# Kernel optimization log

Hardware: AMD Instinct MI355X
Metric: run time of the kernel (lower is better)

## Reference

```python
import jax, jax.numpy as jnp
import numpy as np

B, S, H = 2, 2048, 2048
INTER = 1024
N_ROUTED = 8
ZERO = 4
TOTAL = N_ROUTED + ZERO
TOP_K = 2
SCALE = 1.5


def setup_inputs() -> dict:
    key = jax.random.key(0)
    k0, k1, k2, k3, k4, k5 = jax.random.split(key, 6)
    w = 0.02  # weight init scale
    return {
        "hidden_states": jax.random.normal(k0, (B, S, H), jnp.float32),
        "classifier_w": jax.random.normal(k1, (TOTAL, H), jnp.float32) * w,
        "e_score_correction_bias": jax.random.normal(k2, (TOTAL,), jnp.float32) * w,
        "gate_w": jax.random.normal(k3, (N_ROUTED, INTER, H), jnp.float32) * w,
        "up_w": jax.random.normal(k4, (N_ROUTED, INTER, H), jnp.float32) * w,
        "down_w": jax.random.normal(k5, (N_ROUTED, H, INTER), jnp.float32) * w,
    }


def reference(hidden_states, classifier_w, e_score_correction_bias, gate_w, up_w, down_w):
    x = hidden_states  # [B,S,H]
    total = classifier_w.shape[0]
    n_routed = gate_w.shape[0]

    # --- Router: softmax over all experts, bias only for selection ---
    logits = jnp.einsum('bsh,eh->bse', x, classifier_w)          # [B,S,total]
    probs = jax.nn.softmax(logits, axis=-1)
    biased = probs + e_score_correction_bias
    _, idx = jax.lax.top_k(biased, TOP_K)                         # [B,S,K] int
    rw = jnp.take_along_axis(probs, idx, axis=-1) * SCALE         # unbiased probs as weights

    # Dense per-expert weight via one-hot combine (Equal+Mul+ReduceSum in original)
    w_full = jnp.sum(jax.nn.one_hot(idx, total, dtype=x.dtype) * rw[..., None], axis=-2)  # [B,S,total]

    # --- Compute ALL routed experts densely (matches original op graph) ---
    g = jnp.einsum('bsh,eih->bsei', x, gate_w)                    # [B,S,E,INTER]
    u = jnp.einsum('bsh,eih->bsei', x, up_w)
    act = jax.nn.silu(g) * u
    expert_out = jnp.einsum('bsei,ehi->bseh', act, down_w)        # [B,S,E,H]

    out = jnp.einsum('bse,bseh->bsh', w_full[..., :n_routed], expert_out)
    # Zero (identity) experts pass hidden_states through
    out = out + x * jnp.sum(w_full[..., n_routed:], axis=-1, keepdims=True)
    return out
```

## Files before the change

### kernel.cpp

```cpp
#include <hip/hip_runtime.h>
#include <cstdint>

#define T_TOKENS 4096
#define HDIM 2048
#define IDIM 1024
#define NEXP 8
#define NTOT 12
#define MAX_SLOTS 8320

typedef __bf16 bf16x8_t __attribute__((ext_vector_type(8)));
typedef float f32x4_t __attribute__((ext_vector_type(4)));
typedef unsigned short u16x8_t __attribute__((ext_vector_type(8)));

__device__ __forceinline__ unsigned short f2bf(float f) {
    unsigned int u = __builtin_bit_cast(unsigned int, f);
    u += 0x7fffu + ((u >> 16) & 1u);
    return (unsigned short)(u >> 16);
}
__device__ __forceinline__ float bfu2f(unsigned short u) {
    unsigned int v = ((unsigned int)u) << 16;
    return __builtin_bit_cast(float, v);
}
__device__ __forceinline__ void async16(const unsigned short* g, unsigned short* l) {
    __builtin_amdgcn_global_load_lds(
        (const unsigned int __attribute__((address_space(1)))*)g,
        (unsigned int __attribute__((address_space(3)))*)l,
        16, 0, 0);
}
__device__ __forceinline__ void cvt16(const float* src, unsigned short* dst) {
    f32x4_t f0 = ((const f32x4_t*)src)[0];
    f32x4_t f1 = ((const f32x4_t*)src)[1];
    f32x4_t f2 = ((const f32x4_t*)src)[2];
    f32x4_t f3 = ((const f32x4_t*)src)[3];
    u16x8_t a, b;
#pragma unroll
    for (int j = 0; j < 4; ++j) { a[j] = f2bf(f0[j]); a[4 + j] = f2bf(f1[j]); }
#pragma unroll
    for (int j = 0; j < 4; ++j) { b[j] = f2bf(f2[j]); b[4 + j] = f2bf(f3[j]); }
    ((u16x8_t*)dst)[0] = a;
    ((u16x8_t*)dst)[1] = b;
}

__global__ void init_kernel(int* __restrict__ meta) {
    int i = threadIdx.x;
    if (i < 32) meta[i] = 0;
}

__global__ void noop_kernel() {}

__global__ void router_kernel(const float* __restrict__ x,
                              const float* __restrict__ cw,
                              const float* __restrict__ bias,
                              int* __restrict__ counts,
                              int* __restrict__ tok_e,
                              float* __restrict__ tok_w,
                              float* __restrict__ zero_w) {
    const int token = blockIdx.x;
    const int ln = threadIdx.x;
    const float* xr = x + (size_t)token * HDIM;
    float acc[NTOT];
#pragma unroll
    for (int e = 0; e < NTOT; ++e) acc[e] = 0.f;
    for (int h0 = ln * 4; h0 < HDIM; h0 += 256) {
        f32x4_t xv = *(const f32x4_t*)(xr + h0);
#pragma unroll
        for (int e = 0; e < NTOT; ++e) {
            f32x4_t wv = *(const f32x4_t*)(cw + e * HDIM + h0);
            acc[e] += xv[0] * wv[0] + xv[1] * wv[1] + xv[2] * wv[2] + xv[3] * wv[3];
        }
    }
#pragma unroll
    for (int e = 0; e < NTOT; ++e) {
        float v = acc[e];
#pragma unroll
        for (int s = 32; s > 0; s >>= 1) v += __shfl_xor(v, s, 64);
        acc[e] = v;
    }
    if (ln == 0) {
        float mx = acc[0];
#pragma unroll
        for (int e = 1; e < NTOT; ++e) mx = fmaxf(mx, acc[e]);
        float p[NTOT];
        float sum = 0.f;
#pragma unroll
        for (int e = 0; e < NTOT; ++e) { p[e] = __expf(acc[e] - mx); sum += p[e]; }
        float inv = 1.f / sum;
#pragma unroll
        for (int e = 0; e < NTOT; ++e) p[e] *= inv;
        float b[NTOT];
#pragma unroll
        for (int e = 0; e < NTOT; ++e) b[e] = p[e] + bias[e];
        int i0 = 0; float v0 = b[0];
#pragma unroll
        for (int e = 1; e < NTOT; ++e) if (b[e] > v0) { v0 = b[e]; i0 = e; }
        int i1 = -1; float v1 = -3.0e38f;
#pragma unroll
        for (int e = 0; e < NTOT; ++e) if (e != i0 && b[e] > v1) { v1 = b[e]; i1 = e; }
        if (i1 < 0) i1 = (i0 == 0) ? 1 : 0;
        float w0 = p[i0] * 1.5f, w1 = p[i1] * 1.5f;
        tok_e[2 * token] = i0; tok_e[2 * token + 1] = i1;
        tok_w[2 * token] = w0; tok_w[2 * token + 1] = w1;
        float zw = 0.f;
        if (i0 >= NEXP) zw += w0; else atomicAdd(&counts[i0], 1);
        if (i1 >= NEXP) zw += w1; else atomicAdd(&counts[i1], 1);
        zero_w[token] = zw;
    }
}

__global__ void scan_kernel(const int* __restrict__ counts, int* __restrict__ offs) {
    if (threadIdx.x == 0 && blockIdx.x == 0) {
        int a = 0;
        for (int e = 0; e < NEXP; ++e) {
            offs[e] = a;
            int c = counts[e];
            if (c < 0) c = 0;
            if (c > T_TOKENS) c = T_TOKENS;
            a += c;
        }
        if (a > 2 * T_TOKENS) a = 2 * T_TOKENS;
        offs[NEXP] = a;
    }
}

__global__ void place_kernel(const int* __restrict__ tok_e, const float* __restrict__ tok_w,
                             const int* __restrict__ offs, int* __restrict__ fill,
                             int* __restrict__ token_list, float* __restrict__ slot_w,
                             int* __restrict__ map) {
    int token = blockIdx.x * blockDim.x + threadIdx.x;
    if (token >= T_TOKENS) return;
#pragma unroll
    for (int j = 0; j < 2; ++j) {
        int e = tok_e[2 * token + j];
        int m = -1;
        if (e >= 0 && e < NEXP) {
            int pos = atomicAdd(&fill[e], 1);
            int slot = offs[e] + pos;
            if (slot >= 0 && slot < 2 * T_TOKENS) {
                token_list[slot] = token;
                slot_w[slot] = tok_w[2 * token + j];
                m = slot;
            }
        }
        map[2 * token + j] = m;
    }
}

__launch_bounds__(256, 2)
__global__ void gemm1_kernel(const float* __restrict__ x,
                             const float* __restrict__ gate_w,
                             const float* __restrict__ up_w,
                             const int* __restrict__ offs,
                             const int* __restrict__ token_list,
                             const float* __restrict__ slot_w,
                             unsigned short* __restrict__ act) {
    const int e = blockIdx.z;
    const int off = offs[e];
    int Me = offs[e + 1] - off;
    if (Me < 0) Me = 0;
    if (Me > T_TOKENS) Me = T_TOKENS;
    const int m0 = blockIdx.y * 128;
    if (m0 >= Me) return;
    const int n0 = blockIdx.x * 128;

    __shared__ __align__(16) unsigned short As[128][32];
    __shared__ __align__(16) unsigned short Gs[128][32];
    __shared__ __align__(16) unsigned short Us[128][32];

    const int tid = threadIdx.x;
    const int srow = tid >> 1;
    const int shalf = (tid & 1) * 16;

    int tr = m0 + srow; if (tr >= Me) tr = Me - 1;
    int tok = token_list[off + tr];
    if (tok < 0 || tok >= T_TOKENS) tok = 0;
    const float* aA = x + (size_t)tok * HDIM + shalf;
    const float* aG = gate_w + (size_t)e * IDIM * HDIM + (size_t)(n0 + srow) * HDIM + shalf;
    const float* aU = up_w + (size_t)e * IDIM * HDIM + (size_t)(n0 + srow) * HDIM + shalf;
    unsigned short* lA = &As[srow][shalf];
    unsigned short* lG = &Gs[srow][shalf];
    unsigned short* lU = &Us[srow][shalf];

    const int wv = tid >> 6, ln = tid & 63;
    const int wm = wv & 1, wn = wv >> 1;
    const int fr = ln & 15;
    const int fk = (ln >> 4) * 8;

    f32x4_t accg[4][4] = {};
    f32x4_t accu[4][4] = {};

    for (int k0 = 0; k0 < HDIM; k0 += 32) {
        cvt16(aA + k0, lA);
        cvt16(aG + k0, lG);
        cvt16(aU + k0, lU);
        __syncthreads();
        bf16x8_t af[4], gf[4], uf[4];
#pragma unroll
        for (int t = 0; t < 4; ++t) {
            af[t] = *(const bf16x8_t*)&As[wm * 64 + t * 16 + fr][fk];
            gf[t] = *(const bf16x8_t*)&Gs[wn * 64 + t * 16 + fr][fk];
            uf[t] = *(const bf16x8_t*)&Us[wn * 64 + t * 16 + fr][fk];
        }
#pragma unroll
        for (int mt = 0; mt < 4; ++mt)
#pragma unroll
            for (int nt = 0; nt < 4; ++nt) {
                accg[mt][nt] = __builtin_amdgcn_mfma_f32_16x16x32_bf16(af[mt], gf[nt], accg[mt][nt], 0, 0, 0);
                accu[mt][nt] = __builtin_amdgcn_mfma_f32_16x16x32_bf16(af[mt], uf[nt], accu[mt][nt], 0, 0, 0);
            }
        __syncthreads();
    }

#pragma unroll
    for (int mt = 0; mt < 4; ++mt) {
#pragma unroll
        for (int r = 0; r < 4; ++r) {
            int rloc = wm * 64 + mt * 16 + (ln >> 4) * 4 + r;
            int grow = m0 + rloc;
            if (grow < Me) {
                float w = slot_w[off + grow];
                size_t rb = (size_t)(off + grow) * IDIM + n0;
#pragma unroll
                for (int nt = 0; nt < 4; ++nt) {
                    float g = accg[mt][nt][r];
                    float u = accu[mt][nt][r];
                    float s = g / (1.f + __expf(-g));
                    act[rb + wn * 64 + nt * 16 + fr] = f2bf(s * u * w);
                }
            }
        }
    }
}

__launch_bounds__(256, 2)
__global__ void gemm2_kernel(const unsigned short* __restrict__ act,
                             const float* __restrict__ dwn,
                             const int* __restrict__ offs,
                             unsigned short* __restrict__ dout) {
    const int e = blockIdx.z;
    const int off = offs[e];
    int Me = offs[e + 1] - off;
    if (Me < 0) Me = 0;
    if (Me > T_TOKENS) Me = T_TOKENS;
    const int m0 = blockIdx.y * 128;
    if (m0 >= Me) return;
    const int n0 = blockIdx.x * 128;

    __shared__ __align__(16) unsigned short As[128][32];
    __shared__ __align__(16) unsigned short Bs[128][32];

    const int tid = threadIdx.x;
    const int wv = tid >> 6, ln = tid & 63;

    const int sr0 = wv * 16 + (ln >> 2);
    const int sc = (ln & 3) * 8;
    int ar0 = off + m0 + sr0;      if (ar0 >= MAX_SLOTS) ar0 = MAX_SLOTS - 1;
    int ar1 = off + m0 + 64 + sr0; if (ar1 >= MAX_SLOTS) ar1 = MAX_SLOTS - 1;
    const unsigned short* aA0 = act + (size_t)ar0 * IDIM + sc;
    const unsigned short* aA1 = act + (size_t)ar1 * IDIM + sc;
    unsigned short* lA0 = &As[wv * 16][0];
    unsigned short* lA1 = &As[64 + wv * 16][0];

    const int srow = tid >> 1;
    const int shalf = (tid & 1) * 16;
    const float* aB = dwn + (size_t)e * HDIM * IDIM + (size_t)(n0 + srow) * IDIM + shalf;
    unsigned short* lB = &Bs[srow][shalf];

    const int wm = wv & 1, wn = wv >> 1;
    const int fr = ln & 15;
    const int fk = (ln >> 4) * 8;

    f32x4_t acc[4][4] = {};

    for (int k0 = 0; k0 < IDIM; k0 += 32) {
        async16(aA0 + k0, lA0);
        async16(aA1 + k0, lA1);
        cvt16(aB + k0, lB);
        __syncthreads();
        bf16x8_t af[4], bfr[4];
#pragma unroll
        for (int t = 0; t < 4; ++t) {
            af[t] = *(const bf16x8_t*)&As[wm * 64 + t * 16 + fr][fk];
            bfr[t] = *(const bf16x8_t*)&Bs[wn * 64 + t * 16 + fr][fk];
        }
#pragma unroll
        for (int mt = 0; mt < 4; ++mt)
#pragma unroll
            for (int nt = 0; nt < 4; ++nt)
                acc[mt][nt] = __builtin_amdgcn_mfma_f32_16x16x32_bf16(af[mt], bfr[nt], acc[mt][nt], 0, 0, 0);
        __syncthreads();
    }

#pragma unroll
    for (int mt = 0; mt < 4; ++mt) {
#pragma unroll
        for (int r = 0; r < 4; ++r) {
            int rloc = wm * 64 + mt * 16 + (ln >> 4) * 4 + r;
            int grow = m0 + rloc;
            if (grow < Me) {
                size_t rb = (size_t)(off + grow) * HDIM + n0;
#pragma unroll
                for (int nt = 0; nt < 4; ++nt)
                    dout[rb + wn * 64 + nt * 16 + fr] = f2bf(acc[mt][nt][r]);
            }
        }
    }
}

__global__ void finalize_kernel(const float* __restrict__ x,
                                const unsigned short* __restrict__ dout,
                                const int* __restrict__ map,
                                const float* __restrict__ zero_w,
                                float* __restrict__ out) {
    int gid = blockIdx.x * blockDim.x + threadIdx.x;
    int token = gid >> 8;
    int hg = (gid & 255) * 8;
    int s0 = map[2 * token], s1 = map[2 * token + 1];
    float zw = zero_w[token];
    size_t base = (size_t)token * HDIM + hg;
    f32x4_t x0 = *(const f32x4_t*)(x + base);
    f32x4_t x1 = *(const f32x4_t*)(x + base + 4);
    float o[8];
#pragma unroll
    for (int j = 0; j < 4; ++j) { o[j] = zw * x0[j]; o[4 + j] = zw * x1[j]; }
    if (s0 >= 0 && s0 < 2 * T_TOKENS) {
        u16x8_t d = *(const u16x8_t*)(dout + (size_t)s0 * HDIM + hg);
#pragma unroll
        for (int j = 0; j < 8; ++j) o[j] += bfu2f(d[j]);
    }
    if (s1 >= 0 && s1 < 2 * T_TOKENS) {
        u16x8_t d = *(const u16x8_t*)(dout + (size_t)s1 * HDIM + hg);
#pragma unroll
        for (int j = 0; j < 8; ++j) o[j] += bfu2f(d[j]);
    }
    f32x4_t o0, o1;
#pragma unroll
    for (int j = 0; j < 4; ++j) { o0[j] = o[j]; o1[j] = o[4 + j]; }
    *(f32x4_t*)(out + base) = o0;
    *(f32x4_t*)(out + base + 4) = o1;
}

extern "C" void kernel_launch(void* const* d_in, const int* in_sizes, int n_in,
                              void* d_out, int out_size, void* d_ws, size_t ws_size,
                              hipStream_t stream) {
    const float* x = (const float*)d_in[0];
    const float* cw = (const float*)d_in[1];
    const float* bias = (const float*)d_in[2];
    const float* gw = (const float*)d_in[3];
    const float* uw = (const float*)d_in[4];
    const float* dw = (const float*)d_in[5];
    float* out = (float*)d_out;

    char* ws = (char*)d_ws;
    int* counts = (int*)(ws + 0);
    int* fill = (int*)(ws + 32);
    int* offs = (int*)(ws + 64);
    int* tok_e = (int*)(ws + 128);
    float* tok_w = (float*)(ws + 32896);
    float* zero_w = (float*)(ws + 65664);
    int* map = (int*)(ws + 82048);
    int* token_list = (int*)(ws + 114816);
    float* slot_w = (float*)(ws + 148096);
    unsigned short* act = (unsigned short*)(ws + 181504);
    unsigned short* dout = (unsigned short*)(ws + 181504 + 17039360);
    const size_t needed = 181504ull + 17039360ull + 34078720ull;
    if (ws_size < needed) {
        noop_kernel<<<1, 64, 0, stream>>>();
        return;
    }

    init_kernel<<<1, 64, 0, stream>>>((int*)ws);

    router_kernel<<<T_TOKENS, 64, 0, stream>>>(x, cw, bias, counts, tok_e, tok_w, zero_w);
    scan_kernel<<<1, 64, 0, stream>>>(counts, offs);
    place_kernel<<<(T_TOKENS + 255) / 256, 256, 0, stream>>>(tok_e, tok_w, offs, fill,
                                                             token_list, slot_w, map);
    gemm1_kernel<<<dim3(IDIM / 128, 32, NEXP), 256, 0, stream>>>(x, gw, uw, offs,
                                                                 token_list, slot_w, act);
    gemm2_kernel<<<dim3(HDIM / 128, 32, NEXP), 256, 0, stream>>>(act, dw, offs, dout);
    finalize_kernel<<<(T_TOKENS * HDIM / 8 + 255) / 256, 256, 0, stream>>>(x, dout, map,
                                                                           zero_w, out);
}
```

Measured before the change: 517.9 us.

## Double-buffer LDS staging and shrink M tile to 64 in expert GEMMs

Both expert GEMM kernels now use double-buffered shared memory: the next K slice is loaded from global memory and converted while the current slice feeds the MFMAs, leaving one barrier per iteration. The M tile drops from 128 to 64 rows, with each wave covering 32 columns, and the launch grid grows to match. This should hide global load latency and cut padding waste for experts with few tokens. The cost is lower data reuse per block (the fp32 weights are re-read and re-converted for twice as many M tiles) and more register pressure from prefetched values.

```diff
diff --git a/kernel.cpp b/kernel.cpp
--- a/kernel.cpp
+++ b/kernel.cpp
@@ -11,6 +11,7 @@
 typedef __bf16 bf16x8_t __attribute__((ext_vector_type(8)));
 typedef float f32x4_t __attribute__((ext_vector_type(4)));
 typedef unsigned short u16x8_t __attribute__((ext_vector_type(8)));
+typedef unsigned int u32x4_t __attribute__((ext_vector_type(4)));
 
 __device__ __forceinline__ unsigned short f2bf(float f) {
     unsigned int u = __builtin_bit_cast(unsigned int, f);
@@ -20,25 +21,23 @@
 __device__ __forceinline__ float bfu2f(unsigned short u) {
     unsigned int v = ((unsigned int)u) << 16;
     return __builtin_bit_cast(float, v);
+}
+__device__ __forceinline__ unsigned int pk2(float a, float b) {
+    return (unsigned int)f2bf(a) | ((unsigned int)f2bf(b) << 16);
+}
+__device__ __forceinline__ void pack8(f32x4_t f0, f32x4_t f1, unsigned short* dst) {
+    u32x4_t v;
+    v[0] = pk2(f0[0], f0[1]);
+    v[1] = pk2(f0[2], f0[3]);
+    v[2] = pk2(f1[0], f1[1]);
+    v[3] = pk2(f1[2], f1[3]);
+    *(u32x4_t*)dst = v;
 }
 __device__ __forceinline__ void async16(const unsigned short* g, unsigned short* l) {
     __builtin_amdgcn_global_load_lds(
         (const unsigned int __attribute__((address_space(1)))*)g,
         (unsigned int __attribute__((address_space(3)))*)l,
         16, 0, 0);
-}
-__device__ __forceinline__ void cvt16(const float* src, unsigned short* dst) {
-    f32x4_t f0 = ((const f32x4_t*)src)[0];
-    f32x4_t f1 = ((const f32x4_t*)src)[1];
-    f32x4_t f2 = ((const f32x4_t*)src)[2];
-    f32x4_t f3 = ((const f32x4_t*)src)[3];
-    u16x8_t a, b;
-#pragma unroll
-    for (int j = 0; j < 4; ++j) { a[j] = f2bf(f0[j]); a[4 + j] = f2bf(f1[j]); }
-#pragma unroll
-    for (int j = 0; j < 4; ++j) { b[j] = f2bf(f2[j]); b[4 + j] = f2bf(f3[j]); }
-    ((u16x8_t*)dst)[0] = a;
-    ((u16x8_t*)dst)[1] = b;
 }
 
 __global__ void init_kernel(int* __restrict__ meta) {
@@ -158,52 +157,71 @@
     int Me = offs[e + 1] - off;
     if (Me < 0) Me = 0;
     if (Me > T_TOKENS) Me = T_TOKENS;
-    const int m0 = blockIdx.y * 128;
+    const int m0 = blockIdx.y * 64;
     if (m0 >= Me) return;
     const int n0 = blockIdx.x * 128;
 
-    __shared__ __align__(16) unsigned short As[128][32];
-    __shared__ __align__(16) unsigned short Gs[128][32];
-    __shared__ __align__(16) unsigned short Us[128][32];
+    __shared__ __align__(16) unsigned short As[2][64][32];
+    __shared__ __align__(16) unsigned short Gs[2][128][32];
+    __shared__ __align__(16) unsigned short Us[2][128][32];
 
     const int tid = threadIdx.x;
-    const int srow = tid >> 1;
-    const int shalf = (tid & 1) * 16;
-
-    int tr = m0 + srow; if (tr >= Me) tr = Me - 1;
+    const int arow = tid >> 2;
+    const int acol = (tid & 3) * 8;
+
+    int tr = m0 + arow; if (tr >= Me) tr = Me - 1;
     int tok = token_list[off + tr];
     if (tok < 0 || tok >= T_TOKENS) tok = 0;
-    const float* aA = x + (size_t)tok * HDIM + shalf;
-    const float* aG = gate_w + (size_t)e * IDIM * HDIM + (size_t)(n0 + srow) * HDIM + shalf;
-    const float* aU = up_w + (size_t)e * IDIM * HDIM + (size_t)(n0 + srow) * HDIM + shalf;
-    unsigned short* lA = &As[srow][shalf];
-    unsigned short* lG = &Gs[srow][shalf];
-    unsigned short* lU = &Us[srow][shalf];
+    const float* aA = x + (size_t)tok * HDIM + acol;
+    const float* gb = gate_w + (size_t)e * IDIM * HDIM;
+    const float* ub = up_w + (size_t)e * IDIM * HDIM;
+    const float* aG0 = gb + (size_t)(n0 + arow) * HDIM + acol;
+    const float* aG1 = gb + (size_t)(n0 + 64 + arow) * HDIM + acol;
+    const float* aU0 = ub + (size_t)(n0 + arow) * HDIM + acol;
+    const float* aU1 = ub + (size_t)(n0 + 64 + arow) * HDIM + acol;
 
     const int wv = tid >> 6, ln = tid & 63;
-    const int wm = wv & 1, wn = wv >> 1;
-    const int fr = ln & 15;
-    const int fk = (ln >> 4) * 8;
-
-    f32x4_t accg[4][4] = {};
-    f32x4_t accu[4][4] = {};
-
-    for (int k0 = 0; k0 < HDIM; k0 += 32) {
-        cvt16(aA + k0, lA);
-        cvt16(aG + k0, lG);
-        cvt16(aU + k0, lU);
-        __syncthreads();
-        bf16x8_t af[4], gf[4], uf[4];
-#pragma unroll
-        for (int t = 0; t < 4; ++t) {
-            af[t] = *(const bf16x8_t*)&As[wm * 64 + t * 16 + fr][fk];
-            gf[t] = *(const bf16x8_t*)&Gs[wn * 64 + t * 16 + fr][fk];
-            uf[t] = *(const bf16x8_t*)&Us[wn * 64 + t * 16 + fr][fk];
+    const int fr = ln & 15, fk = (ln >> 4) * 8;
+
+    f32x4_t accg[4][2] = {};
+    f32x4_t accu[4][2] = {};
+
+    auto stage = [&](int k, int b) {
+        const int kc = k * 32;
+        f32x4_t a0 = *(const f32x4_t*)(aA + kc);
+        f32x4_t a1 = *(const f32x4_t*)(aA + kc + 4);
+        f32x4_t g00 = *(const f32x4_t*)(aG0 + kc);
+        f32x4_t g01 = *(const f32x4_t*)(aG0 + kc + 4);
+        f32x4_t g10 = *(const f32x4_t*)(aG1 + kc);
+        f32x4_t g11 = *(const f32x4_t*)(aG1 + kc + 4);
+        f32x4_t u00 = *(const f32x4_t*)(aU0 + kc);
+        f32x4_t u01 = *(const f32x4_t*)(aU0 + kc + 4);
+        f32x4_t u10 = *(const f32x4_t*)(aU1 + kc);
+        f32x4_t u11 = *(const f32x4_t*)(aU1 + kc + 4);
+        pack8(a0, a1, &As[b][arow][acol]);
+        pack8(g00, g01, &Gs[b][arow][acol]);
+        pack8(g10, g11, &Gs[b][64 + arow][acol]);
+        pack8(u00, u01, &Us[b][arow][acol]);
+        pack8(u10, u11, &Us[b][64 + arow][acol]);
+    };
+
+    stage(0, 0);
+    __syncthreads();
+    for (int k = 0; k < HDIM / 32; ++k) {
+        const int b = k & 1;
+        if (k < HDIM / 32 - 1) stage(k + 1, b ^ 1);
+        bf16x8_t af[4], gf[2], uf[2];
+#pragma unroll
+        for (int t = 0; t < 4; ++t) af[t] = *(const bf16x8_t*)&As[b][t * 16 + fr][fk];
+#pragma unroll
+        for (int t = 0; t < 2; ++t) {
+            gf[t] = *(const bf16x8_t*)&Gs[b][wv * 32 + t * 16 + fr][fk];
+            uf[t] = *(const bf16x8_t*)&Us[b][wv * 32 + t * 16 + fr][fk];
         }
 #pragma unroll
         for (int mt = 0; mt < 4; ++mt)
 #pragma unroll
-            for (int nt = 0; nt < 4; ++nt) {
+            for (int nt = 0; nt < 2; ++nt) {
                 accg[mt][nt] = __builtin_amdgcn_mfma_f32_16x16x32_bf16(af[mt], gf[nt], accg[mt][nt], 0, 0, 0);
                 accu[mt][nt] = __builtin_amdgcn_mfma_f32_16x16x32_bf16(af[mt], uf[nt], accu[mt][nt], 0, 0, 0);
             }
@@ -214,17 +232,17 @@
     for (int mt = 0; mt < 4; ++mt) {
 #pragma unroll
         for (int r = 0; r < 4; ++r) {
-            int rloc = wm * 64 + mt * 16 + (ln >> 4) * 4 + r;
+            int rloc = mt * 16 + (ln >> 4) * 4 + r;
             int grow = m0 + rloc;
             if (grow < Me) {
                 float w = slot_w[off + grow];
-                size_t rb = (size_t)(off + grow) * IDIM + n0;
-#pragma unroll
-                for (int nt = 0; nt < 4; ++nt) {
+                size_t rb = (size_t)(off + grow) * IDIM + n0 + wv * 32;
+#pragma unroll
+                for (int nt = 0; nt < 2; ++nt) {
                     float g = accg[mt][nt][r];
                     float u = accu[mt][nt][r];
                     float s = g / (1.f + __expf(-g));
-                    act[rb + wn * 64 + nt * 16 + fr] = f2bf(s * u * w);
+                    act[rb + nt * 16 + fr] = f2bf(s * u * w);
                 }
             }
         }
@@ -241,66 +259,73 @@
     int Me = offs[e + 1] - off;
     if (Me < 0) Me = 0;
     if (Me > T_TOKENS) Me = T_TOKENS;
-    const int m0 = blockIdx.y * 128;
+    const int m0 = blockIdx.y * 64;
     if (m0 >= Me) return;
     const int n0 = blockIdx.x * 128;
 
-    __shared__ __align__(16) unsigned short As[128][32];
-    __shared__ __align__(16) unsigned short Bs[128][32];
+    __shared__ __align__(16) unsigned short As[2][64][32];
+    __shared__ __align__(16) unsigned short Bs[2][128][32];
 
     const int tid = threadIdx.x;
     const int wv = tid >> 6, ln = tid & 63;
 
-    const int sr0 = wv * 16 + (ln >> 2);
+    const int sr = wv * 16 + (ln >> 2);
     const int sc = (ln & 3) * 8;
-    int ar0 = off + m0 + sr0;      if (ar0 >= MAX_SLOTS) ar0 = MAX_SLOTS - 1;
-    int ar1 = off + m0 + 64 + sr0; if (ar1 >= MAX_SLOTS) ar1 = MAX_SLOTS - 1;
-    const unsigned short* aA0 = act + (size_t)ar0 * IDIM + sc;
-    const unsigned short* aA1 = act + (size_t)ar1 * IDIM + sc;
-    unsigned short* lA0 = &As[wv * 16][0];
-    unsigned short* lA1 = &As[64 + wv * 16][0];
-
-    const int srow = tid >> 1;
-    const int shalf = (tid & 1) * 16;
-    const float* aB = dwn + (size_t)e * HDIM * IDIM + (size_t)(n0 + srow) * IDIM + shalf;
-    unsigned short* lB = &Bs[srow][shalf];
-
-    const int wm = wv & 1, wn = wv >> 1;
-    const int fr = ln & 15;
-    const int fk = (ln >> 4) * 8;
-
-    f32x4_t acc[4][4] = {};
-
-    for (int k0 = 0; k0 < IDIM; k0 += 32) {
-        async16(aA0 + k0, lA0);
-        async16(aA1 + k0, lA1);
-        cvt16(aB + k0, lB);
+    int ar = off + m0 + sr; if (ar >= MAX_SLOTS) ar = MAX_SLOTS - 1;
+    const unsigned short* aA = act + (size_t)ar * IDIM + sc;
+    unsigned short* lA0 = &As[0][wv * 16][0];
+    unsigned short* lA1 = &As[1][wv * 16][0];
+
+    const int brow = tid >> 2;
+    const int bcol = (tid & 3) * 8;
+    const float* bb = dwn + (size_t)e * HDIM * IDIM;
+    const float* aB0 = bb + (size_t)(n0 + brow) * IDIM + bcol;
+    const float* aB1 = bb + (size_t)(n0 + 64 + brow) * IDIM + bcol;
+
+    const int fr = ln & 15, fk = (ln >> 4) * 8;
+
+    f32x4_t acc[4][2] = {};
+
+    auto stage = [&](int k, int b) {
+        const int kc = k * 32;
+        async16(aA + kc, b ? lA1 : lA0);
+        f32x4_t b00 = *(const f32x4_t*)(aB0 + kc);
+        f32x4_t b01 = *(const f32x4_t*)(aB0 + kc + 4);
+        f32x4_t b10 = *(const f32x4_t*)(aB1 + kc);
+        f32x4_t b11 = *(const f32x4_t*)(aB1 + kc + 4);
+        pack8(b00, b01, &Bs[b][brow][bcol]);
+        pack8(b10, b11, &Bs[b][64 + brow][bcol]);
+    };
+
+    stage(0, 0);
+    __syncthreads();
+    for (int k = 0; k < IDIM / 32; ++k) {
+        const int b = k & 1;
+        if (k < IDIM / 32 - 1) stage(k + 1, b ^ 1);
+        bf16x8_t af[4], bf[2];
+#pragma unroll
+        for (int t = 0; t < 4; ++t) af[t] = *(const bf16x8_t*)&As[b][t * 16 + fr][fk];
+#pragma unroll
+        for (int t = 0; t < 2; ++t) bf[t] = *(const bf16x8_t*)&Bs[b][wv * 32 + t * 16 + fr][fk];
+#pragma unroll
+        for (int mt = 0; mt < 4; ++mt)
+#pragma unroll
+            for (int nt = 0; nt < 2; ++nt)
+                acc[mt][nt] = __builtin_amdgcn_mfma_f32_16x16x32_bf16(af[mt], bf[nt], acc[mt][nt], 0, 0, 0);
         __syncthreads();
-        bf16x8_t af[4], bfr[4];
-#pragma unroll
-        for (int t = 0; t < 4; ++t) {
-            af[t] = *(const bf16x8_t*)&As[wm * 64 + t * 16 + fr][fk];
-            bfr[t] = *(const bf16x8_t*)&Bs[wn * 64 + t * 16 + fr][fk];
-        }
-#pragma unroll
-        for (int mt = 0; mt < 4; ++mt)
-#pragma unroll
-            for (int nt = 0; nt < 4; ++nt)
-                acc[mt][nt] = __builtin_amdgcn_mfma_f32_16x16x32_bf16(af[mt], bfr[nt], acc[mt][nt], 0, 0, 0);
-        __syncthreads();
     }
 
 #pragma unroll
     for (int mt = 0; mt < 4; ++mt) {
 #pragma unroll
         for (int r = 0; r < 4; ++r) {
-            int rloc = wm * 64 + mt * 16 + (ln >> 4) * 4 + r;
+            int rloc = mt * 16 + (ln >> 4) * 4 + r;
             int grow = m0 + rloc;
             if (grow < Me) {
-                size_t rb = (size_t)(off + grow) * HDIM + n0;
-#pragma unroll
-                for (int nt = 0; nt < 4; ++nt)
-                    dout[rb + wn * 64 + nt * 16 + fr] = f2bf(acc[mt][nt][r]);
+                size_t rb = (size_t)(off + grow) * HDIM + n0 + wv * 32;
+#pragma unroll
+                for (int nt = 0; nt < 2; ++nt)
+                    dout[rb + nt * 16 + fr] = f2bf(acc[mt][nt][r]);
             }
         }
     }
@@ -374,9 +399,10 @@
     scan_kernel<<<1, 64, 0, stream>>>(counts, offs);
     place_kernel<<<(T_TOKENS + 255) / 256, 256, 0, stream>>>(tok_e, tok_w, offs, fill,
                                                              token_list, slot_w, map);
-    gemm1_kernel<<<dim3(IDIM / 128, 32, NEXP), 256, 0, stream>>>(x, gw, uw, offs,
-                                                                 token_list, slot_w, act);
-    gemm2_kernel<<<dim3(HDIM / 128, 32, NEXP), 256, 0, stream>>>(act, dw, offs, dout);
+    gemm1_kernel<<<dim3(IDIM / 128, T_TOKENS / 64, NEXP), 256, 0, stream>>>(
+        x, gw, uw, offs, token_list, slot_w, act);
+    gemm2_kernel<<<dim3(HDIM / 128, T_TOKENS / 64, NEXP), 256, 0, stream>>>(
+        act, dw, offs, dout);
     finalize_kernel<<<(T_TOKENS * HDIM / 8 + 255) / 256, 256, 0, stream>>>(x, dout, map,
                                                                            zero_w, out);
 }
```

Result: slower. 534.8 us (+3.3%).
